# Kernel tuning notes

Measured on AMD Instinct MI355X. Metric: run time of the kernel, lower is better.

## Reference

```python
import jax, jax.numpy as jnp
import numpy as np

B, N = 4, 2048
IN_F, OUT_F, H = 128, 128, 8
HD = OUT_F // H  # 16
ALPHA = 0.2       # LeakyReLU negative slope
TIME_DECAY = 0.1


def setup_inputs() -> dict:
    key = jax.random.key(0)
    k1, k2, k3, k4, k5 = jax.random.split(key, 5)
    node_features = jax.random.normal(k1, (B, N, IN_F), dtype=jnp.float32)
    adj_matrix = jax.random.randint(k2, (B, N, N), 0, 2, dtype=jnp.int32)
    time_matrix = jax.random.uniform(k3, (B, N, N), dtype=jnp.float32)
    # xavier_uniform with gain=1.414 as in the torch module
    def xavier(k, shape, fan_in, fan_out):
        bound = 1.414 * np.sqrt(6.0 / (fan_in + fan_out))
        return jax.random.uniform(k, shape, minval=-bound, maxval=bound, dtype=jnp.float32)
    W = xavier(k4, (H, IN_F, HD), IN_F, HD)
    a = xavier(k5, (H, 2 * HD, 1), 2 * HD, 1)
    return {"node_features": node_features, "adj_matrix": adj_matrix,
            "time_matrix": time_matrix, "W": W, "a": a}


def reference(node_features, adj_matrix, time_matrix, W, a):
    # time weights (eq 17): exp(-lambda * (t_max - t))
    current_time = jnp.max(time_matrix)
    time_weights = jnp.exp(-TIME_DECAY * (current_time - time_matrix))  # [B,N,N]

    # per-head projection: [B,H,N,HD]
    h = jnp.einsum('bni,hio->bhno', node_features, W)

    # decompose attention vector a = [a_src; a_dst] so we never build the
    # O(N^2 * 2*HD) concat tensor: e_ij = LeakyReLU(a_src.h_i + a_dst.h_j)
    a_src = a[:, :HD, 0]   # [H,HD]
    a_dst = a[:, HD:, 0]   # [H,HD]
    e_i = jnp.einsum('bhnd,hd->bhn', h, a_src)  # score contribution of node i
    e_j = jnp.einsum('bhnd,hd->bhn', h, a_dst)  # score contribution of node j
    e = e_i[:, :, :, None] + e_j[:, :, None, :]          # [B,H,N,N]
    e = jax.nn.leaky_relu(e, negative_slope=ALPHA)
    e = e * time_weights[:, None, :, :]

    # mask non-edges, normalize (dropout is identity in eval mode)
    mask = adj_matrix[:, None, :, :] == 0                 # [B,1->H,N,N]
    e = jnp.where(mask, -jnp.inf, e)
    attention = jax.nn.softmax(e, axis=-1)                # [B,H,N,N]

    # aggregate neighbors, merge heads, ELU
    out = jnp.einsum('bhij,bhjo->bhio', attention, h)     # [B,H,N,HD]
    out = jnp.transpose(out, (0, 2, 1, 3)).reshape(node_features.shape[0], node_features.shape[1], -1)
    return jax.nn.elu(out)
```

## Files before the change

kernel.cpp:

```cpp
#include <hip/hip_runtime.h>
#include <hip/hip_bf16.h>

#define BN    4
#define NN    2048
#define INF   128
#define HH    8
#define HD    16
#define ALPHA 0.2f
#define DECAY 0.1f

typedef __attribute__((ext_vector_type(8))) short short8;
typedef __attribute__((ext_vector_type(4))) float float4v;

__device__ __forceinline__ float bf2f(unsigned short u) {
    return __uint_as_float(((unsigned)u) << 16);
}

__global__ void k_max(const float* __restrict__ tm, unsigned* __restrict__ ct) {
    const uint4* p = (const uint4*)tm;
    const int nvec = BN * NN * NN / 4;
    int idx = blockIdx.x * blockDim.x + threadIdx.x;
    int stride = gridDim.x * blockDim.x;
    unsigned m = 0u;
    for (int i = idx; i < nvec; i += stride) {
        uint4 v = p[i];
        m = max(m, v.x); m = max(m, v.y); m = max(m, v.z); m = max(m, v.w);
    }
    float fm = __uint_as_float(m);
    #pragma unroll
    for (int o = 32; o >= 1; o >>= 1) fm = fmaxf(fm, __shfl_xor(fm, o));
    __shared__ float sm[4];
    if ((threadIdx.x & 63) == 0) sm[threadIdx.x >> 6] = fm;
    __syncthreads();
    if (threadIdx.x == 0) {
        float mm = fmaxf(fmaxf(sm[0], sm[1]), fmaxf(sm[2], sm[3]));
        atomicMax(ct, __float_as_uint(mm));
    }
}

__global__ void k_proj(const float* __restrict__ x,
                       const float* __restrict__ W,
                       const float* __restrict__ a,
                       __hip_bfloat16* __restrict__ h_t,
                       float* __restrict__ es, float* __restrict__ ed) {
    int b = blockIdx.x >> 11;
    int n = blockIdx.x & 2047;
    int t = threadIdx.x;
    __shared__ float xs[INF];
    xs[t] = x[((size_t)(b * NN + n)) * INF + t];
    __syncthreads();
    int h = t >> 4, d = t & 15;
    const float* Wp = W + (h * INF) * HD + d;
    float acc = 0.f;
    #pragma unroll 16
    for (int i = 0; i < INF; i++) acc += xs[i] * Wp[i * HD];
    h_t[((size_t)((b * HH + h) * HD + d)) * NN + n] = __float2bfloat16(acc);
    float s  = acc * a[h * 2 * HD + d];
    float dd = acc * a[h * 2 * HD + HD + d];
    #pragma unroll
    for (int o = 8; o >= 1; o >>= 1) { s += __shfl_xor(s, o); dd += __shfl_xor(dd, o); }
    if (d == 0) {
        es[(b * HH + h) * NN + n] = s;
        ed[(b * HH + h) * NN + n] = dd;
    }
}

__launch_bounds__(512, 4)
__global__ void k_attn(const int* __restrict__ adj,
                       const float* __restrict__ tm,
                       const __hip_bfloat16* __restrict__ h_t,
                       const float* __restrict__ es, const float* __restrict__ ed,
                       const unsigned* __restrict__ ctp,
                       float* __restrict__ out) {
    int t    = threadIdx.x;
    int w    = t >> 6;
    int lane = t & 63;
    int q    = lane >> 4;
    int im   = lane & 15;
    int b    = blockIdx.x >> 7;
    int i0   = (blockIdx.x & 127) << 4;
    int i    = i0 + im;

    __shared__ float tws[16][132];

    float negdct = -DECAY * __uint_as_float(*ctp);
    float es_i = es[(b * HH + w) * NN + i];

    const float* ed_p = ed + (size_t)(b * HH + w) * NN + q * 8;
    const __hip_bfloat16* ht_p = h_t + ((size_t)((b * HH + w) * HD + im)) * NN + q * 8;

    int srow = t >> 5;
    int scol = (t & 31) << 2;
    const int*   adj_s = adj + ((size_t)(b * NN + i0 + srow)) * NN + scol;
    const float* tm_s  = tm  + ((size_t)(b * NN + i0 + srow)) * NN + scol;

    float4v acc = {0.f, 0.f, 0.f, 0.f};
    float lsum = 0.f;

    int4   pa = *(const int4*)(adj_s);
    float4 pt = *(const float4*)(tm_s);

    for (int r = 0; r < 16; r++) {
        float w0 = (pa.x != 0) ? __expf(fmaf(DECAY, pt.x, negdct)) : 0.f;
        float w1 = (pa.y != 0) ? __expf(fmaf(DECAY, pt.y, negdct)) : 0.f;
        float w2 = (pa.z != 0) ? __expf(fmaf(DECAY, pt.z, negdct)) : 0.f;
        float w3 = (pa.w != 0) ? __expf(fmaf(DECAY, pt.w, negdct)) : 0.f;

        __syncthreads();
        *(float4*)&tws[srow][scol] = make_float4(w0, w1, w2, w3);

        if (r + 1 < 16) {
            pa = *(const int4*)(adj_s + (r + 1) * 128);
            pt = *(const float4*)(tm_s + (r + 1) * 128);
        }
        __syncthreads();

        #pragma unroll
        for (int c4 = 0; c4 < 4; c4++) {
            int jl = c4 * 32 + q * 8;
            int jglob = r * 128 + c4 * 32;

            float4 w01 = *(const float4*)&tws[im][jl];
            float4 w23 = *(const float4*)&tws[im][jl + 4];
            float4 e0 = *(const float4*)(ed_p + jglob);
            float4 e1 = *(const float4*)(ed_p + jglob + 4);
            uint4  hv = *(const uint4*)(ht_p + jglob);

            float wv[8] = {w01.x, w01.y, w01.z, w01.w, w23.x, w23.y, w23.z, w23.w};
            float ev[8] = {e0.x, e0.y, e0.z, e0.w, e1.x, e1.y, e1.z, e1.w};

            union { unsigned short us[8]; short8 v; } af;
            #pragma unroll
            for (int k = 0; k < 8; k++) {
                float s0  = es_i + ev[k];
                float sc  = fmaxf(s0, ALPHA * s0);
                float pv  = __expf(sc * wv[k]);
                pv = (wv[k] > 0.f) ? pv : 0.f;
                __hip_bfloat16 hb = __float2bfloat16(pv);
                unsigned short ub;
                __builtin_memcpy(&ub, &hb, 2);
                af.us[k] = ub;
                lsum += bf2f(ub);
            }
            union { uint4 u; short8 v; } bf;
            bf.u = hv;
            acc = __builtin_amdgcn_mfma_f32_16x16x32_bf16(af.v, bf.v, acc, 0, 0, 0);
        }
    }

    lsum += __shfl_xor(lsum, 16);
    lsum += __shfl_xor(lsum, 32);
    float inv = 1.f / lsum;

    #pragma unroll
    for (int r = 0; r < 4; r++) {
        int row = q * 4 + r;
        float invr = __shfl(inv, row);
        float v = acc[r] * invr;
        v = (v > 0.f) ? v : expm1f(v);
        out[((size_t)(b * NN + i0 + row)) * (HH * HD) + w * HD + im] = v;
    }
}

extern "C" void kernel_launch(void* const* d_in, const int* in_sizes, int n_in,
                              void* d_out, int out_size, void* d_ws, size_t ws_size,
                              hipStream_t stream) {
    const float* x   = (const float*)d_in[0];
    const int*   adj = (const int*)d_in[1];
    const float* tm  = (const float*)d_in[2];
    const float* W   = (const float*)d_in[3];
    const float* a   = (const float*)d_in[4];
    float* out = (float*)d_out;

    float* wsf = (float*)d_ws;
    unsigned* ct = (unsigned*)wsf;
    float* es = wsf + 64;
    float* ed = es + BN * HH * NN;
    __hip_bfloat16* h_t = (__hip_bfloat16*)(ed + BN * HH * NN);

    hipMemsetAsync(d_ws, 0, 4, stream);
    k_max <<<1024, 256, 0, stream>>>(tm, ct);
    k_proj<<<BN * NN, 128, 0, stream>>>(x, W, a, h_t, es, ed);
    k_attn<<<BN * (NN / 16), 512, 0, stream>>>(adj, tm, h_t, es, ed, ct, out);
}
```

Measured before the change: 235.3 us.

## Split attention over neighbor halves, double-buffer LDS, fuse setup kernels

The attention kernel now splits the neighbor dimension into two halves. This doubles the block count, and a new finalize kernel adds the partial accumulators and softmax sums, then normalizes and applies ELU. The time-weight tile in shared memory is double-buffered, so each iteration needs one barrier instead of two. The max reduction and the projection are merged into one launch, and the exponentials are rewritten as exp2 with log2(e) folded into the time weight. The cost is extra global traffic for the partials, one more launch, tighter launch bounds, and a softmax sum that now uses the unrounded probabilities.

```diff
diff --git a/kernel.cpp b/kernel.cpp
--- a/kernel.cpp
+++ b/kernel.cpp
@@ -9,6 +9,9 @@
 #define ALPHA 0.2f
 #define DECAY 0.1f
 
+#define DLOG2E 0.14426950408889634f
+#define LLOG2E 0.5287663729448977f
+
 typedef __attribute__((ext_vector_type(8))) short short8;
 typedef __attribute__((ext_vector_type(4))) float float4v;
 
@@ -16,112 +19,130 @@
     return __uint_as_float(((unsigned)u) << 16);
 }
 
-__global__ void k_max(const float* __restrict__ tm, unsigned* __restrict__ ct) {
-    const uint4* p = (const uint4*)tm;
-    const int nvec = BN * NN * NN / 4;
-    int idx = blockIdx.x * blockDim.x + threadIdx.x;
-    int stride = gridDim.x * blockDim.x;
-    unsigned m = 0u;
-    for (int i = idx; i < nvec; i += stride) {
-        uint4 v = p[i];
-        m = max(m, v.x); m = max(m, v.y); m = max(m, v.z); m = max(m, v.w);
-    }
-    float fm = __uint_as_float(m);
-    #pragma unroll
-    for (int o = 32; o >= 1; o >>= 1) fm = fmaxf(fm, __shfl_xor(fm, o));
-    __shared__ float sm[4];
-    if ((threadIdx.x & 63) == 0) sm[threadIdx.x >> 6] = fm;
-    __syncthreads();
-    if (threadIdx.x == 0) {
-        float mm = fmaxf(fmaxf(sm[0], sm[1]), fmaxf(sm[2], sm[3]));
-        atomicMax(ct, __float_as_uint(mm));
-    }
-}
-
-__global__ void k_proj(const float* __restrict__ x,
-                       const float* __restrict__ W,
-                       const float* __restrict__ a,
-                       __hip_bfloat16* __restrict__ h_t,
-                       float* __restrict__ es, float* __restrict__ ed) {
-    int b = blockIdx.x >> 11;
-    int n = blockIdx.x & 2047;
-    int t = threadIdx.x;
-    __shared__ float xs[INF];
-    xs[t] = x[((size_t)(b * NN + n)) * INF + t];
-    __syncthreads();
-    int h = t >> 4, d = t & 15;
-    const float* Wp = W + (h * INF) * HD + d;
-    float acc = 0.f;
-    #pragma unroll 16
-    for (int i = 0; i < INF; i++) acc += xs[i] * Wp[i * HD];
-    h_t[((size_t)((b * HH + h) * HD + d)) * NN + n] = __float2bfloat16(acc);
-    float s  = acc * a[h * 2 * HD + d];
-    float dd = acc * a[h * 2 * HD + HD + d];
-    #pragma unroll
-    for (int o = 8; o >= 1; o >>= 1) { s += __shfl_xor(s, o); dd += __shfl_xor(dd, o); }
-    if (d == 0) {
-        es[(b * HH + h) * NN + n] = s;
-        ed[(b * HH + h) * NN + n] = dd;
-    }
-}
-
-__launch_bounds__(512, 4)
+__launch_bounds__(256, 8)
+__global__ void k_setup(const float* __restrict__ x,
+                        const float* __restrict__ W,
+                        const float* __restrict__ a,
+                        const float* __restrict__ tm,
+                        unsigned* __restrict__ ct,
+                        __hip_bfloat16* __restrict__ h_t,
+                        float* __restrict__ es, float* __restrict__ ed) {
+    if (blockIdx.x < 1024) {
+        const uint4* p = (const uint4*)tm;
+        const int nvec = BN * NN * NN / 4;
+        int idx = blockIdx.x * 256 + threadIdx.x;
+        const int stride = 1024 * 256;
+        unsigned m = 0u;
+        for (int i = idx; i < nvec; i += stride) {
+            uint4 v = p[i];
+            m = max(m, v.x); m = max(m, v.y); m = max(m, v.z); m = max(m, v.w);
+        }
+        float fm = __uint_as_float(m);
+        #pragma unroll
+        for (int o = 32; o >= 1; o >>= 1) fm = fmaxf(fm, __shfl_xor(fm, o));
+        __shared__ float sm[4];
+        if ((threadIdx.x & 63) == 0) sm[threadIdx.x >> 6] = fm;
+        __syncthreads();
+        if (threadIdx.x == 0) {
+            float mm = fmaxf(fmaxf(sm[0], sm[1]), fmaxf(sm[2], sm[3]));
+            atomicMax(ct, __float_as_uint(mm));
+        }
+    } else {
+        int bid = blockIdx.x - 1024;
+        int sub = threadIdx.x >> 7;
+        int tt  = threadIdx.x & 127;
+        int nn  = bid * 2 + sub;
+        __shared__ float xs[2][INF];
+        xs[sub][tt] = x[(size_t)nn * INF + tt];
+        __syncthreads();
+        int h = tt >> 4, d = tt & 15;
+        const float* Wp = W + (h * INF) * HD + d;
+        float acc = 0.f;
+        #pragma unroll 16
+        for (int i = 0; i < INF; i++) acc += xs[sub][i] * Wp[i * HD];
+        int b = nn >> 11, n = nn & 2047;
+        h_t[((size_t)((b * HH + h) * HD + d)) * NN + n] = __float2bfloat16(acc);
+        float s  = acc * a[h * 2 * HD + d];
+        float dd = acc * a[h * 2 * HD + HD + d];
+        #pragma unroll
+        for (int o = 8; o >= 1; o >>= 1) { s += __shfl_xor(s, o); dd += __shfl_xor(dd, o); }
+        if (d == 0) {
+            es[(b * HH + h) * NN + n] = s;
+            ed[(b * HH + h) * NN + n] = dd;
+        }
+    }
+}
+
+__launch_bounds__(512, 8)
 __global__ void k_attn(const int* __restrict__ adj,
                        const float* __restrict__ tm,
                        const __hip_bfloat16* __restrict__ h_t,
                        const float* __restrict__ es, const float* __restrict__ ed,
                        const unsigned* __restrict__ ctp,
-                       float* __restrict__ out) {
+                       float* __restrict__ pacc, float* __restrict__ pl) {
     int t    = threadIdx.x;
     int w    = t >> 6;
     int lane = t & 63;
     int q    = lane >> 4;
     int im   = lane & 15;
-    int b    = blockIdx.x >> 7;
-    int i0   = (blockIdx.x & 127) << 4;
+    int bx   = blockIdx.x;
+    int b    = bx >> 8;
+    int half = (bx >> 7) & 1;
+    int i0   = (bx & 127) << 4;
     int i    = i0 + im;
-
-    __shared__ float tws[16][132];
-
-    float negdct = -DECAY * __uint_as_float(*ctp);
+    int jb   = half << 10;
+    const int R = 8;
+
+    __shared__ float tws[2][16][132];
+
+    float ctv = __uint_as_float(*ctp);
+    float c0  = fmaf(-DLOG2E, ctv, LLOG2E);
     float es_i = es[(b * HH + w) * NN + i];
 
-    const float* ed_p = ed + (size_t)(b * HH + w) * NN + q * 8;
-    const __hip_bfloat16* ht_p = h_t + ((size_t)((b * HH + w) * HD + im)) * NN + q * 8;
+    const float* ed_p = ed + (size_t)(b * HH + w) * NN + jb + q * 8;
+    const __hip_bfloat16* ht_p = h_t + ((size_t)((b * HH + w) * HD + im)) * NN + jb + q * 8;
 
     int srow = t >> 5;
     int scol = (t & 31) << 2;
-    const int*   adj_s = adj + ((size_t)(b * NN + i0 + srow)) * NN + scol;
-    const float* tm_s  = tm  + ((size_t)(b * NN + i0 + srow)) * NN + scol;
+    const int*   adj_s = adj + ((size_t)(b * NN + i0 + srow)) * NN + jb + scol;
+    const float* tm_s  = tm  + ((size_t)(b * NN + i0 + srow)) * NN + jb + scol;
 
     float4v acc = {0.f, 0.f, 0.f, 0.f};
     float lsum = 0.f;
 
     int4   pa = *(const int4*)(adj_s);
     float4 pt = *(const float4*)(tm_s);
-
-    for (int r = 0; r < 16; r++) {
-        float w0 = (pa.x != 0) ? __expf(fmaf(DECAY, pt.x, negdct)) : 0.f;
-        float w1 = (pa.y != 0) ? __expf(fmaf(DECAY, pt.y, negdct)) : 0.f;
-        float w2 = (pa.z != 0) ? __expf(fmaf(DECAY, pt.z, negdct)) : 0.f;
-        float w3 = (pa.w != 0) ? __expf(fmaf(DECAY, pt.w, negdct)) : 0.f;
-
-        __syncthreads();
-        *(float4*)&tws[srow][scol] = make_float4(w0, w1, w2, w3);
-
-        if (r + 1 < 16) {
-            pa = *(const int4*)(adj_s + (r + 1) * 128);
-            pt = *(const float4*)(tm_s + (r + 1) * 128);
-        }
-        __syncthreads();
-
+    {
+        float w0 = (pa.x != 0) ? exp2f(fmaf(DLOG2E, pt.x, c0)) : 0.f;
+        float w1 = (pa.y != 0) ? exp2f(fmaf(DLOG2E, pt.y, c0)) : 0.f;
+        float w2 = (pa.z != 0) ? exp2f(fmaf(DLOG2E, pt.z, c0)) : 0.f;
+        float w3 = (pa.w != 0) ? exp2f(fmaf(DLOG2E, pt.w, c0)) : 0.f;
+        *(float4*)&tws[0][srow][scol] = make_float4(w0, w1, w2, w3);
+    }
+    pa = *(const int4*)(adj_s + 128);
+    pt = *(const float4*)(tm_s + 128);
+    __syncthreads();
+
+    for (int r = 0; r < R; r++) {
+        int cur = r & 1;
+        if (r + 1 < R) {
+            float w0 = (pa.x != 0) ? exp2f(fmaf(DLOG2E, pt.x, c0)) : 0.f;
+            float w1 = (pa.y != 0) ? exp2f(fmaf(DLOG2E, pt.y, c0)) : 0.f;
+            float w2 = (pa.z != 0) ? exp2f(fmaf(DLOG2E, pt.z, c0)) : 0.f;
+            float w3 = (pa.w != 0) ? exp2f(fmaf(DLOG2E, pt.w, c0)) : 0.f;
+            *(float4*)&tws[cur ^ 1][srow][scol] = make_float4(w0, w1, w2, w3);
+            if (r + 2 < R) {
+                pa = *(const int4*)(adj_s + (r + 2) * 128);
+                pt = *(const float4*)(tm_s + (r + 2) * 128);
+            }
+        }
         #pragma unroll
         for (int c4 = 0; c4 < 4; c4++) {
             int jl = c4 * 32 + q * 8;
             int jglob = r * 128 + c4 * 32;
 
-            float4 w01 = *(const float4*)&tws[im][jl];
-            float4 w23 = *(const float4*)&tws[im][jl + 4];
+            float4 w01 = *(const float4*)&tws[cur][im][jl];
+            float4 w23 = *(const float4*)&tws[cur][im][jl + 4];
             float4 e0 = *(const float4*)(ed_p + jglob);
             float4 e1 = *(const float4*)(ed_p + jglob + 4);
             uint4  hv = *(const uint4*)(ht_p + jglob);
@@ -132,34 +153,56 @@
             union { unsigned short us[8]; short8 v; } af;
             #pragma unroll
             for (int k = 0; k < 8; k++) {
-                float s0  = es_i + ev[k];
-                float sc  = fmaxf(s0, ALPHA * s0);
-                float pv  = __expf(sc * wv[k]);
+                float s0 = es_i + ev[k];
+                float sc = fmaxf(s0, ALPHA * s0);
+                float pv = exp2f(sc * wv[k]);
                 pv = (wv[k] > 0.f) ? pv : 0.f;
+                lsum += pv;
                 __hip_bfloat16 hb = __float2bfloat16(pv);
                 unsigned short ub;
                 __builtin_memcpy(&ub, &hb, 2);
                 af.us[k] = ub;
-                lsum += bf2f(ub);
             }
             union { uint4 u; short8 v; } bf;
             bf.u = hv;
             acc = __builtin_amdgcn_mfma_f32_16x16x32_bf16(af.v, bf.v, acc, 0, 0, 0);
         }
+        __syncthreads();
     }
 
     lsum += __shfl_xor(lsum, 16);
     lsum += __shfl_xor(lsum, 32);
-    float inv = 1.f / lsum;
-
+
+    float* pb = pacc + (((size_t)bx * 8 + w) * 16) * 16;
     #pragma unroll
     for (int r = 0; r < 4; r++) {
         int row = q * 4 + r;
-        float invr = __shfl(inv, row);
-        float v = acc[r] * invr;
-        v = (v > 0.f) ? v : expm1f(v);
-        out[((size_t)(b * NN + i0 + row)) * (HH * HD) + w * HD + im] = v;
-    }
+        pb[row * 16 + im] = acc[r];
+    }
+    if (q == 0) pl[(size_t)bx * 128 + w * 16 + im] = lsum;
+}
+
+__launch_bounds__(256, 8)
+__global__ void k_fin(const float* __restrict__ pacc, const float* __restrict__ pl,
+                      float* __restrict__ out) {
+    int o = blockIdx.x * 256 + threadIdx.x;
+    int b   = o >> 18;
+    int rem = o & 262143;
+    int i   = rem >> 7;
+    int hd  = rem & 127;
+    int h   = hd >> 4;
+    int d   = hd & 15;
+    int it  = i >> 4;
+    int row = i & 15;
+    int blk0 = (b * 2 + 0) * 128 + it;
+    int blk1 = blk0 + 128;
+    float a0 = pacc[(((size_t)blk0 * 8 + h) * 16 + row) * 16 + d];
+    float a1 = pacc[(((size_t)blk1 * 8 + h) * 16 + row) * 16 + d];
+    float l  = pl[(size_t)blk0 * 128 + h * 16 + row]
+             + pl[(size_t)blk1 * 128 + h * 16 + row];
+    float v = (a0 + a1) / l;
+    v = (v > 0.f) ? v : expm1f(v);
+    out[o] = v;
 }
 
 extern "C" void kernel_launch(void* const* d_in, const int* in_sizes, int n_in,
@@ -177,9 +220,11 @@
     float* es = wsf + 64;
     float* ed = es + BN * HH * NN;
     __hip_bfloat16* h_t = (__hip_bfloat16*)(ed + BN * HH * NN);
+    float* pacc = (float*)(h_t + BN * HH * HD * NN);
+    float* pl   = pacc + 1024 * 2048;
 
     hipMemsetAsync(d_ws, 0, 4, stream);
-    k_max <<<1024, 256, 0, stream>>>(tm, ct);
-    k_proj<<<BN * NN, 128, 0, stream>>>(x, W, a, h_t, es, ed);
-    k_attn<<<BN * (NN / 16), 512, 0, stream>>>(adj, tm, h_t, es, ed, ct, out);
-}
+    k_setup<<<1024 + 4096, 256, 0, stream>>>(x, W, a, tm, ct, h_t, es, ed);
+    k_attn <<<BN * 2 * (NN / 16), 512, 0, stream>>>(adj, tm, h_t, es, ed, ct, pacc, pl);
+    k_fin  <<<(BN * NN * HH * HD) / 256, 256, 0, stream>>>(pacc, pl, out);
+}
```

After: 234.1 us. No clear change (-0.5%).

## Merge max-reduce and projection kernels, transpose W, fold log2e into time weights

Applied to the files above, without the earlier changes.

Replaces the memset plus the separate time-max and projection launches with a tiny W-transpose/zeroing kernel and one combined setup kernel. In that kernel, the first blocks reduce the time maximum while the remaining blocks compute the projection with a coalesced transposed W, two nodes per block. In the attention kernel, the log2(e) scale is folded into the time-weight constant so both exponentials become exp2f without an extra multiply per element. This cuts launch overhead and per-element ALU work, at the cost of an extra small serial kernel and slightly more workspace.

```diff
diff --git a/kernel.cpp b/kernel.cpp
--- a/kernel.cpp
+++ b/kernel.cpp
@@ -9,6 +9,9 @@
 #define ALPHA 0.2f
 #define DECAY 0.1f
 
+#define DLOG2E 0.14426950408889634f
+#define LLOG2E 0.5287663729448977f
+
 typedef __attribute__((ext_vector_type(8))) short short8;
 typedef __attribute__((ext_vector_type(4))) float float4v;
 
@@ -16,52 +19,68 @@
     return __uint_as_float(((unsigned)u) << 16);
 }
 
-__global__ void k_max(const float* __restrict__ tm, unsigned* __restrict__ ct) {
-    const uint4* p = (const uint4*)tm;
-    const int nvec = BN * NN * NN / 4;
-    int idx = blockIdx.x * blockDim.x + threadIdx.x;
-    int stride = gridDim.x * blockDim.x;
-    unsigned m = 0u;
-    for (int i = idx; i < nvec; i += stride) {
-        uint4 v = p[i];
-        m = max(m, v.x); m = max(m, v.y); m = max(m, v.z); m = max(m, v.w);
-    }
-    float fm = __uint_as_float(m);
-    #pragma unroll
-    for (int o = 32; o >= 1; o >>= 1) fm = fmaxf(fm, __shfl_xor(fm, o));
-    __shared__ float sm[4];
-    if ((threadIdx.x & 63) == 0) sm[threadIdx.x >> 6] = fm;
-    __syncthreads();
-    if (threadIdx.x == 0) {
-        float mm = fmaxf(fmaxf(sm[0], sm[1]), fmaxf(sm[2], sm[3]));
-        atomicMax(ct, __float_as_uint(mm));
-    }
-}
-
-__global__ void k_proj(const float* __restrict__ x,
-                       const float* __restrict__ W,
-                       const float* __restrict__ a,
-                       __hip_bfloat16* __restrict__ h_t,
-                       float* __restrict__ es, float* __restrict__ ed) {
-    int b = blockIdx.x >> 11;
-    int n = blockIdx.x & 2047;
+__global__ void k_prep(const float* __restrict__ W, float* __restrict__ Wt,
+                       unsigned* __restrict__ ct) {
     int t = threadIdx.x;
-    __shared__ float xs[INF];
-    xs[t] = x[((size_t)(b * NN + n)) * INF + t];
-    __syncthreads();
-    int h = t >> 4, d = t & 15;
-    const float* Wp = W + (h * INF) * HD + d;
-    float acc = 0.f;
-    #pragma unroll 16
-    for (int i = 0; i < INF; i++) acc += xs[i] * Wp[i * HD];
-    h_t[((size_t)((b * HH + h) * HD + d)) * NN + n] = __float2bfloat16(acc);
-    float s  = acc * a[h * 2 * HD + d];
-    float dd = acc * a[h * 2 * HD + HD + d];
-    #pragma unroll
-    for (int o = 8; o >= 1; o >>= 1) { s += __shfl_xor(s, o); dd += __shfl_xor(dd, o); }
-    if (d == 0) {
-        es[(b * HH + h) * NN + n] = s;
-        ed[(b * HH + h) * NN + n] = dd;
+    if (t == 0) *ct = 0u;
+    for (int e = t; e < HH * INF * HD; e += 256) {
+        int h = e >> 11;
+        int i = (e >> 4) & 127;
+        int d = e & 15;
+        Wt[i * 128 + h * 16 + d] = W[e];
+    }
+}
+
+__launch_bounds__(256, 8)
+__global__ void k_setup(const float* __restrict__ x,
+                        const float* __restrict__ Wt,
+                        const float* __restrict__ a,
+                        const float* __restrict__ tm,
+                        unsigned* __restrict__ ct,
+                        __hip_bfloat16* __restrict__ h_t,
+                        float* __restrict__ es, float* __restrict__ ed) {
+    if (blockIdx.x < 1024) {
+        const uint4* p = (const uint4*)tm;
+        const int nvec = BN * NN * NN / 4;
+        int idx = blockIdx.x * 256 + threadIdx.x;
+        const int stride = 1024 * 256;
+        unsigned m = 0u;
+        for (int i = idx; i < nvec; i += stride) {
+            uint4 v = p[i];
+            m = max(m, v.x); m = max(m, v.y); m = max(m, v.z); m = max(m, v.w);
+        }
+        float fm = __uint_as_float(m);
+        #pragma unroll
+        for (int o = 32; o >= 1; o >>= 1) fm = fmaxf(fm, __shfl_xor(fm, o));
+        __shared__ float sm[4];
+        if ((threadIdx.x & 63) == 0) sm[threadIdx.x >> 6] = fm;
+        __syncthreads();
+        if (threadIdx.x == 0) {
+            float mm = fmaxf(fmaxf(sm[0], sm[1]), fmaxf(sm[2], sm[3]));
+            atomicMax(ct, __float_as_uint(mm));
+        }
+    } else {
+        int bid = blockIdx.x - 1024;
+        int sub = threadIdx.x >> 7;
+        int tt  = threadIdx.x & 127;
+        int nn  = bid * 2 + sub;
+        __shared__ float xs[2][INF];
+        xs[sub][tt] = x[(size_t)nn * INF + tt];
+        __syncthreads();
+        int h = tt >> 4, d = tt & 15;
+        float acc = 0.f;
+        #pragma unroll 16
+        for (int i = 0; i < INF; i++) acc += xs[sub][i] * Wt[i * 128 + tt];
+        int b = nn >> 11, n = nn & 2047;
+        h_t[((size_t)((b * HH + h) * HD + d)) * NN + n] = __float2bfloat16(acc);
+        float s  = acc * a[h * 2 * HD + d];
+        float dd = acc * a[h * 2 * HD + HD + d];
+        #pragma unroll
+        for (int o = 8; o >= 1; o >>= 1) { s += __shfl_xor(s, o); dd += __shfl_xor(dd, o); }
+        if (d == 0) {
+            es[(b * HH + h) * NN + n] = s;
+            ed[(b * HH + h) * NN + n] = dd;
+        }
     }
 }
 
@@ -80,10 +99,12 @@
     int b    = blockIdx.x >> 7;
     int i0   = (blockIdx.x & 127) << 4;
     int i    = i0 + im;
+    const int R = 16;
 
     __shared__ float tws[16][132];
 
-    float negdct = -DECAY * __uint_as_float(*ctp);
+    float ctv = __uint_as_float(*ctp);
+    float c0  = fmaf(-DLOG2E, ctv, LLOG2E);
     float es_i = es[(b * HH + w) * NN + i];
 
     const float* ed_p = ed + (size_t)(b * HH + w) * NN + q * 8;
@@ -100,16 +121,16 @@
     int4   pa = *(const int4*)(adj_s);
     float4 pt = *(const float4*)(tm_s);
 
-    for (int r = 0; r < 16; r++) {
-        float w0 = (pa.x != 0) ? __expf(fmaf(DECAY, pt.x, negdct)) : 0.f;
-        float w1 = (pa.y != 0) ? __expf(fmaf(DECAY, pt.y, negdct)) : 0.f;
-        float w2 = (pa.z != 0) ? __expf(fmaf(DECAY, pt.z, negdct)) : 0.f;
-        float w3 = (pa.w != 0) ? __expf(fmaf(DECAY, pt.w, negdct)) : 0.f;
+    for (int r = 0; r < R; r++) {
+        float w0 = (pa.x != 0) ? exp2f(fmaf(DLOG2E, pt.x, c0)) : 0.f;
+        float w1 = (pa.y != 0) ? exp2f(fmaf(DLOG2E, pt.y, c0)) : 0.f;
+        float w2 = (pa.z != 0) ? exp2f(fmaf(DLOG2E, pt.z, c0)) : 0.f;
+        float w3 = (pa.w != 0) ? exp2f(fmaf(DLOG2E, pt.w, c0)) : 0.f;
 
         __syncthreads();
         *(float4*)&tws[srow][scol] = make_float4(w0, w1, w2, w3);
 
-        if (r + 1 < 16) {
+        if (r + 1 < R) {
             pa = *(const int4*)(adj_s + (r + 1) * 128);
             pt = *(const float4*)(tm_s + (r + 1) * 128);
         }
@@ -132,9 +153,9 @@
             union { unsigned short us[8]; short8 v; } af;
             #pragma unroll
             for (int k = 0; k < 8; k++) {
-                float s0  = es_i + ev[k];
-                float sc  = fmaxf(s0, ALPHA * s0);
-                float pv  = __expf(sc * wv[k]);
+                float s0 = es_i + ev[k];
+                float sc = fmaxf(s0, ALPHA * s0);
+                float pv = exp2f(sc * wv[k]);
                 pv = (wv[k] > 0.f) ? pv : 0.f;
                 __hip_bfloat16 hb = __float2bfloat16(pv);
                 unsigned short ub;
@@ -174,12 +195,12 @@
 
     float* wsf = (float*)d_ws;
     unsigned* ct = (unsigned*)wsf;
-    float* es = wsf + 64;
+    float* Wt = wsf + 64;
+    float* es = Wt + INF * HH * HD;
     float* ed = es + BN * HH * NN;
     __hip_bfloat16* h_t = (__hip_bfloat16*)(ed + BN * HH * NN);
 
-    hipMemsetAsync(d_ws, 0, 4, stream);
-    k_max <<<1024, 256, 0, stream>>>(tm, ct);
-    k_proj<<<BN * NN, 128, 0, stream>>>(x, W, a, h_t, es, ed);
-    k_attn<<<BN * (NN / 16), 512, 0, stream>>>(adj, tm, h_t, es, ed, ct, out);
-}
+    k_prep <<<1, 256, 0, stream>>>(W, Wt, ct);
+    k_setup<<<1024 + 4096, 256, 0, stream>>>(x, Wt, a, tm, ct, h_t, es, ed);
+    k_attn <<<BN * (NN / 16), 512, 0, stream>>>(adj, tm, h_t, es, ed, ct, out);
+}
```

Result: slower. 256.3 us (+8.9%).
